# Optimization experiments

Hardware: AMD Instinct MI355X
Metric: run time of the kernel (lower is better)

The kernel has to match this reference:

```python
import jax, jax.numpy as jnp
import numpy as np
import math

B, L, S, E, D = 32, 2048, 2048, 64, 64

def setup_inputs() -> dict:
    key = jax.random.key(0)
    kq, kk, kv = jax.random.split(key, 3)
    return {
        "queries": jax.random.normal(kq, (B, L, E), dtype=jnp.float32),
        "keys":    jax.random.normal(kk, (B, S, E), dtype=jnp.float32),
        "values":  jax.random.normal(kv, (B, S, D), dtype=jnp.float32),
    }

def reference(queries, keys, values):
    # scale = 1/sqrt(E) since self.scale is None
    scale = 1.0 / math.sqrt(queries.shape[-1])
    # unfused QK^T -> softmax -> V (dropout is identity at inference)
    scores = jnp.einsum('ble,bse->bls', queries, keys)  # [B,L,S]
    # mask_flag branch not taken because L == S (matches torch code path)
    A = jax.nn.softmax(scale * scores, axis=-1)
    V = jnp.einsum('bls,bsd->bld', A, values)  # [B,L,D]
    return V
```

## Files before the change

kernel.cpp:

```cpp
#include <hip/hip_runtime.h>
#include <hip/hip_bf16.h>


#define B_ 32
#define L_ 2048
#define S_ 2048
#define E_ 64
#define D_ 64
#define BQ 128
#define NIMG 32
#define IMG_BYTES 16384
#define NCHUNK 32
#define NBUF 4

typedef __attribute__((ext_vector_type(8))) short bf16x8;
typedef __attribute__((ext_vector_type(16))) float f32x16;
typedef __attribute__((ext_vector_type(4))) unsigned u32x4;

__device__ __forceinline__ unsigned short f2b(float f) {
  unsigned u = __builtin_bit_cast(unsigned, f);
  u += 0x7fff + ((u >> 16) & 1);
  return (unsigned short)(u >> 16);
}

__device__ __forceinline__ unsigned pk2(float a, float b) {
#if defined(__has_builtin) && __has_builtin(__builtin_amdgcn_cvt_pk_bf16_f32)
  typedef __bf16 b2 __attribute__((ext_vector_type(2)));
  b2 t = __builtin_amdgcn_cvt_pk_bf16_f32(a, b);
  return __builtin_bit_cast(unsigned, t);
#else
  return (unsigned)f2b(a) | ((unsigned)f2b(b) << 16);
#endif
}

__device__ __forceinline__ float fexp2(float x) {
#if defined(__has_builtin) && __has_builtin(__builtin_amdgcn_exp2f)
  return __builtin_amdgcn_exp2f(x);
#else
  return exp2f(x);
#endif
}

__device__ __forceinline__ void cp16(const void* g, void* lbase) {
#if defined(__has_builtin) && __has_builtin(__builtin_amdgcn_global_load_lds)
  typedef const __attribute__((address_space(1))) void gvoid;
  typedef __attribute__((address_space(3))) void lvoid;
  __builtin_amdgcn_global_load_lds((gvoid*)g, (lvoid*)lbase, 16, 0, 0);
#endif
}

__device__ __forceinline__ void wait_ge(const volatile int* p, int want) {
  while (*p < want) __builtin_amdgcn_s_sleep(1);
}

__global__ __launch_bounds__(256) void prepass(
    const float* __restrict__ K, const float* __restrict__ V,
    char* __restrict__ ws) {
  const int tid  = threadIdx.x;
  const int lane = tid & 63;
  const int quad = lane >> 4;
  const int qb0  = quad & 1;
  const int qb1  = (quad >> 1) & 1;

  const int b  = blockIdx.x >> 5;
  const int c  = blockIdx.x & 31;
  const int s0 = c * 64;

  const float* Kb = K + (long)b * S_ * E_;
  const float* Vb = V + (long)b * S_ * D_;
  short* img = (short*)(ws + (size_t)blockIdx.x * IMG_BYTES);

#pragma unroll
  for (int it = 0; it < 4; ++it) {
    const int i  = tid + it * 256;
    const int s  = i >> 4;
    const int c4 = (i & 15) << 2;

    float4 kv = *(const float4*)(Kb + (long)(s0 + s) * E_ + c4);
    {
      int g = (c4 >> 3) ^ (s & 7);
      *(uint2*)&img[s * 64 + g * 8 + (c4 & 7)] = make_uint2(pk2(kv.x, kv.y), pk2(kv.z, kv.w));
    }

    float4 vv = *(const float4*)(Vb + (long)(s0 + s) * D_ + c4);
    float a0 = vv.x, a1 = vv.y, a2 = vv.z, a3 = vv.w;
    float s0f = qb1 ? a0 : a2;
    float s1f = qb1 ? a1 : a3;
    float r0  = __shfl_xor(s0f, 32);
    float r1  = __shfl_xor(s1f, 32);
    float b0 = qb1 ? r0 : a0;
    float b1 = qb1 ? r1 : a1;
    float b2 = qb1 ? a2 : r0;
    float b3 = qb1 ? a3 : r1;
    float t0 = qb0 ? b0 : b1;
    float t1 = qb0 ? b2 : b3;
    float u0 = __shfl_xor(t0, 16);
    float u1 = __shfl_xor(t1, 16);
    float w0 = qb0 ? u0 : b0;
    float w1 = qb0 ? b1 : u0;
    float w2 = qb0 ? u1 : b2;
    float w3 = qb0 ? b3 : u1;
    const int base = s - quad;
    const int d    = c4 + quad;
    int g = (base >> 3) ^ (d & 7);
    *(uint2*)&img[4096 + d * 64 + g * 8 + (base & 7)] = make_uint2(pk2(w0, w1), pk2(w2, w3));
  }
}

__global__ __launch_bounds__(512, 4) void attn_fwd(
    const float* __restrict__ Q, const char* __restrict__ ws,
    float* __restrict__ O) {
  __shared__ __align__(16) char smem[65536 + 1024 + 64];
  float* Obuf = (float*)smem;
  float* ML   = (float*)(smem + 65536);
  int*   sync = (int*)(smem + 66560);

  const int tid  = threadIdx.x;
  const int lane = tid & 63;
  const int wv   = tid >> 6;
  const int l31  = lane & 31;
  const int h    = lane >> 5;
  const int qg   = wv >> 1;
  const int kh   = wv & 1;

  const int b  = blockIdx.x >> 4;
  const int q0 = (blockIdx.x & 15) * BQ;

  const float SCALE2 = 0.125f * 1.44269504088896340736f;
  const char* img0 = ws + (size_t)b * ((size_t)NIMG * IMG_BYTES);

  if (tid < 8) sync[tid] = 0;
  __syncthreads();

  if (wv < 4) {
    const char* img = img0 + (size_t)wv * IMG_BYTES;
#pragma unroll
    for (int j = 0; j < 16; ++j)
      cp16(img + j * 1024 + lane * 16, smem + wv * 16384 + j * 1024);
  }

  bf16x8 qf[4];
  {
    const float* qrow = Q + ((long)b * L_ + q0 + qg * 32 + l31) * E_;
#pragma unroll
    for (int ke = 0; ke < 4; ++ke) {
      const float* sp = qrow + ke * 16 + h * 8;
      float4 x = *(const float4*)(sp);
      float4 y = *(const float4*)(sp + 4);
      u32x4 uu = { pk2(x.x * SCALE2, x.y * SCALE2), pk2(x.z * SCALE2, x.w * SCALE2),
                   pk2(y.x * SCALE2, y.y * SCALE2), pk2(y.z * SCALE2, y.w * SCALE2) };
      qf[ke] = __builtin_bit_cast(bf16x8, uu);
    }
  }

  if (wv < 4) {
    asm volatile("s_waitcnt vmcnt(0)" ::: "memory");
    if (lane == 0) ((volatile int*)sync)[wv] = 1;
  }

  int pl = l31;
  {
    const int blk = (pl >> 2) & 3;
    if (blk == 1) pl += 4;
    else if (blk == 2) pl -= 4;
  }

  const int kb = (kh << 12) + (pl << 7) + ((h ^ (pl & 7)) << 4);
  const int vb = 8192 + (l31 << 7) + (((kh * 4 + h) ^ (l31 & 7)) << 4);

  f32x16 o[2];
#pragma unroll
  for (int mt = 0; mt < 2; ++mt)
#pragma unroll
    for (int r = 0; r < 16; ++r) o[mt][r] = 0.f;
  float lrun = 0.f;

  for (int t = 0; t < NCHUNK; ++t) {
    const int s = t & 3;
    wait_ge((volatile int*)&sync[s], (t >> 2) + 1);
    asm volatile("" ::: "memory");

    const int bufb = s << 14;
    const int kbuf = kb ^ bufb;
    const int vbuf = vb ^ bufb;

    bf16x8 kf[4];
#pragma unroll
    for (int ke = 0; ke < 4; ++ke)
      kf[ke] = *(const bf16x8*)(smem + (kbuf ^ (ke << 5)));
    f32x16 acc;
#pragma unroll
    for (int r = 0; r < 16; ++r) acc[r] = 0.f;
#pragma unroll
    for (int ke = 0; ke < 4; ++ke)
      acc = __builtin_amdgcn_mfma_f32_32x32x16_bf16(kf[ke], qf[ke], acc, 0, 0, 0);

    u32x4 f0, f1;
#pragma unroll
    for (int g = 0; g < 4; ++g) {
      float p0 = fexp2(acc[2 * g]);
      float p1 = fexp2(acc[2 * g + 1]);
      lrun += p0 + p1;
      f0[g] = pk2(p0, p1);
      float p2 = fexp2(acc[8 + 2 * g]);
      float p3 = fexp2(acc[8 + 2 * g + 1]);
      lrun += p2 + p3;
      f1[g] = pk2(p2, p3);
    }
    bf16x8 pf0 = __builtin_bit_cast(bf16x8, f0);
    bf16x8 pf1 = __builtin_bit_cast(bf16x8, f1);

#pragma unroll
    for (int mt = 0; mt < 2; ++mt) {
      bf16x8 vf0 = *(const bf16x8*)(smem + (vbuf ^ (mt << 12)));
      o[mt] = __builtin_amdgcn_mfma_f32_32x32x16_bf16(vf0, pf0, o[mt], 0, 0, 0);
      bf16x8 vf1 = *(const bf16x8*)(smem + (vbuf ^ (mt << 12) ^ (1 << 5)));
      o[mt] = __builtin_amdgcn_mfma_f32_32x32x16_bf16(vf1, pf1, o[mt], 0, 0, 0);
    }

    asm volatile("s_waitcnt lgkmcnt(0)" ::: "memory");
    if (lane == 0) atomicAdd(&sync[4 + s], 1);

    const int tp = t + 4;
    if (tp < NCHUNK && (tp & 7) == wv) {
      const int sp_ = tp & 3;
      wait_ge((volatile int*)&sync[4 + sp_], (tp >> 2) * 8);
      asm volatile("" ::: "memory");
      const char* img = img0 + (size_t)tp * IMG_BYTES;
#pragma unroll
      for (int j = 0; j < 16; ++j)
        cp16(img + j * 1024 + lane * 16, smem + sp_ * 16384 + j * 1024);
      asm volatile("s_waitcnt vmcnt(0)" ::: "memory");
      if (lane == 0) ((volatile int*)sync)[sp_] = (tp >> 2) + 1;
    }
  }

  float lt = lrun + __shfl_xor(lrun, 32);

  if (lane < 32)
    ML[(qg * 2 + kh) * 32 + l31] = lt;
  __syncthreads();

  const float inv = 1.f / (lt + ML[(qg * 2 + (kh ^ 1)) * 32 + l31]);
  const int q = qg * 32 + l31;

  if (kh == 1) {
#pragma unroll
    for (int mt = 0; mt < 2; ++mt)
#pragma unroll
      for (int r = 0; r < 16; ++r) {
        const int d = mt * 32 + (r & 3) + 8 * (r >> 2) + 4 * h;
        Obuf[q * 68 + d] = o[mt][r];
      }
  }
  __syncthreads();

  if (kh == 0) {
#pragma unroll
    for (int mt = 0; mt < 2; ++mt)
#pragma unroll
      for (int r = 0; r < 16; ++r) {
        const int d = mt * 32 + (r & 3) + 8 * (r >> 2) + 4 * h;
        Obuf[q * 68 + d] = (o[mt][r] + Obuf[q * 68 + d]) * inv;
      }
  }
  __syncthreads();

  {
    const int qq = tid >> 2;
    const int dh = (tid & 3) * 16;
    float* orow = O + ((long)b * L_ + q0 + qq) * D_ + dh;
    const float* src = &Obuf[qq * 68 + dh];
#pragma unroll
    for (int j = 0; j < 4; ++j)
      *(float4*)(orow + j * 4) = *(const float4*)(src + j * 4);
  }
}

extern "C" void kernel_launch(void* const* d_in, const int* in_sizes, int n_in,
                              void* d_out, int out_size, void* d_ws, size_t ws_size,
                              hipStream_t stream) {
  const float* Q = (const float*)d_in[0];
  const float* K = (const float*)d_in[1];
  const float* V = (const float*)d_in[2];
  float* O = (float*)d_out;

  prepass<<<dim3(B_ * NIMG), dim3(256), 0, stream>>>(K, V, (char*)d_ws);
  attn_fwd<<<dim3(B_ * (L_ / BQ)), dim3(512), 0, stream>>>(Q, (const char*)d_ws, O);
}
```

Baseline: 150.2 us.

## Replace flag-based 4-slot LDS pipeline with barrier double buffering and smaller blocks

Swaps the spin-wait, flag-and-atomic producer/consumer scheme with 4 LDS slots for a simple double buffer. Every wave prefetches its share of the next K/V chunk at the top of each iteration, and a __syncthreads closes the iteration. The query tile drops from 128 to 64 rows with 256-thread blocks, which halves LDS use and doubles the block count to raise occupancy and remove polling overhead. The cost is a full block barrier per chunk and only one chunk of prefetch distance, so global-to-LDS latency may be less well hidden.

```diff
diff --git a/kernel.cpp b/kernel.cpp
--- a/kernel.cpp
+++ b/kernel.cpp
@@ -7,11 +7,10 @@
 #define S_ 2048
 #define E_ 64
 #define D_ 64
-#define BQ 128
+#define BQ 64
 #define NIMG 32
 #define IMG_BYTES 16384
 #define NCHUNK 32
-#define NBUF 4
 
 typedef __attribute__((ext_vector_type(8))) short bf16x8;
 typedef __attribute__((ext_vector_type(16))) float f32x16;
@@ -47,10 +46,6 @@
   typedef __attribute__((address_space(3))) void lvoid;
   __builtin_amdgcn_global_load_lds((gvoid*)g, (lvoid*)lbase, 16, 0, 0);
 #endif
-}
-
-__device__ __forceinline__ void wait_ge(const volatile int* p, int want) {
-  while (*p < want) __builtin_amdgcn_s_sleep(1);
 }
 
 __global__ __launch_bounds__(256) void prepass(
@@ -107,13 +102,12 @@
   }
 }
 
-__global__ __launch_bounds__(512, 4) void attn_fwd(
+__global__ __launch_bounds__(256, 4) void attn_fwd(
     const float* __restrict__ Q, const char* __restrict__ ws,
     float* __restrict__ O) {
-  __shared__ __align__(16) char smem[65536 + 1024 + 64];
+  __shared__ __align__(16) char smem[32768 + 512];
   float* Obuf = (float*)smem;
-  float* ML   = (float*)(smem + 65536);
-  int*   sync = (int*)(smem + 66560);
+  float* ML   = (float*)(smem + 32768);
 
   const int tid  = threadIdx.x;
   const int lane = tid & 63;
@@ -123,21 +117,15 @@
   const int qg   = wv >> 1;
   const int kh   = wv & 1;
 
-  const int b  = blockIdx.x >> 4;
-  const int q0 = (blockIdx.x & 15) * BQ;
+  const int b  = blockIdx.x >> 5;
+  const int q0 = (blockIdx.x & 31) * BQ;
 
   const float SCALE2 = 0.125f * 1.44269504088896340736f;
   const char* img0 = ws + (size_t)b * ((size_t)NIMG * IMG_BYTES);
 
-  if (tid < 8) sync[tid] = 0;
-  __syncthreads();
-
-  if (wv < 4) {
-    const char* img = img0 + (size_t)wv * IMG_BYTES;
-#pragma unroll
-    for (int j = 0; j < 16; ++j)
-      cp16(img + j * 1024 + lane * 16, smem + wv * 16384 + j * 1024);
-  }
+#pragma unroll
+  for (int j = 0; j < 4; ++j)
+    cp16(img0 + (wv * 4 + j) * 1024 + lane * 16, smem + (wv * 4 + j) * 1024);
 
   bf16x8 qf[4];
   {
@@ -153,11 +141,6 @@
     }
   }
 
-  if (wv < 4) {
-    asm volatile("s_waitcnt vmcnt(0)" ::: "memory");
-    if (lane == 0) ((volatile int*)sync)[wv] = 1;
-  }
-
   int pl = l31;
   {
     const int blk = (pl >> 2) & 3;
@@ -175,19 +158,24 @@
     for (int r = 0; r < 16; ++r) o[mt][r] = 0.f;
   float lrun = 0.f;
 
+  __syncthreads();
+
   for (int t = 0; t < NCHUNK; ++t) {
-    const int s = t & 3;
-    wait_ge((volatile int*)&sync[s], (t >> 2) + 1);
-    asm volatile("" ::: "memory");
-
-    const int bufb = s << 14;
-    const int kbuf = kb ^ bufb;
-    const int vbuf = vb ^ bufb;
+    const int slot = t & 1;
+    const int bufb = slot << 14;
+
+    if (t + 1 < NCHUNK) {
+      const char* img = img0 + (size_t)(t + 1) * IMG_BYTES;
+      const int ob = (slot ^ 1) << 14;
+#pragma unroll
+      for (int j = 0; j < 4; ++j)
+        cp16(img + (wv * 4 + j) * 1024 + lane * 16, smem + ob + (wv * 4 + j) * 1024);
+    }
 
     bf16x8 kf[4];
 #pragma unroll
     for (int ke = 0; ke < 4; ++ke)
-      kf[ke] = *(const bf16x8*)(smem + (kbuf ^ (ke << 5)));
+      kf[ke] = *(const bf16x8*)(smem + (kb ^ bufb ^ (ke << 5)));
     f32x16 acc;
 #pragma unroll
     for (int r = 0; r < 16; ++r) acc[r] = 0.f;
@@ -212,27 +200,13 @@
 
 #pragma unroll
     for (int mt = 0; mt < 2; ++mt) {
-      bf16x8 vf0 = *(const bf16x8*)(smem + (vbuf ^ (mt << 12)));
+      bf16x8 vf0 = *(const bf16x8*)(smem + (vb ^ bufb ^ (mt << 12)));
       o[mt] = __builtin_amdgcn_mfma_f32_32x32x16_bf16(vf0, pf0, o[mt], 0, 0, 0);
-      bf16x8 vf1 = *(const bf16x8*)(smem + (vbuf ^ (mt << 12) ^ (1 << 5)));
+      bf16x8 vf1 = *(const bf16x8*)(smem + (vb ^ bufb ^ (mt << 12) ^ (1 << 5)));
       o[mt] = __builtin_amdgcn_mfma_f32_32x32x16_bf16(vf1, pf1, o[mt], 0, 0, 0);
     }
 
-    asm volatile("s_waitcnt lgkmcnt(0)" ::: "memory");
-    if (lane == 0) atomicAdd(&sync[4 + s], 1);
-
-    const int tp = t + 4;
-    if (tp < NCHUNK && (tp & 7) == wv) {
-      const int sp_ = tp & 3;
-      wait_ge((volatile int*)&sync[4 + sp_], (tp >> 2) * 8);
-      asm volatile("" ::: "memory");
-      const char* img = img0 + (size_t)tp * IMG_BYTES;
-#pragma unroll
-      for (int j = 0; j < 16; ++j)
-        cp16(img + j * 1024 + lane * 16, smem + sp_ * 16384 + j * 1024);
-      asm volatile("s_waitcnt vmcnt(0)" ::: "memory");
-      if (lane == 0) ((volatile int*)sync)[sp_] = (tp >> 2) + 1;
-    }
+    __syncthreads();
   }
 
   float lt = lrun + __shfl_xor(lrun, 32);
@@ -286,5 +260,5 @@
   float* O = (float*)d_out;
 
   prepass<<<dim3(B_ * NIMG), dim3(256), 0, stream>>>(K, V, (char*)d_ws);
-  attn_fwd<<<dim3(B_ * (L_ / BQ)), dim3(512), 0, stream>>>(Q, (const char*)d_ws, O);
-}
+  attn_fwd<<<dim3(B_ * (L_ / BQ)), dim3(256), 0, stream>>>(Q, (const char*)d_ws, O);
+}
```

Result: faster. 143.1 us (-4.7%).
